# Kernel tuning notes

Measured on AMD Instinct MI355X. Metric: run time of the kernel, lower is better.

## Reference

```python
import jax, jax.numpy as jnp
import numpy as np

N, F, H, D = 4096, 128, 8, 8  # nodes, in_feat, head_num, att_embedding_size
EDGE_PROB = 0.01
NEG_INF = -1e10  # original uses -10e9 * (1 - A)


def setup_inputs() -> dict:
    key = jax.random.key(0)
    k1, k2, k3, k4, k5 = jax.random.split(key, 5)
    X = jax.random.normal(k1, (N, F), dtype=jnp.float32)
    # binary dense adjacency with self-loops (faithful to the dense-mask GAT formulation)
    A = (jax.random.uniform(k2, (N, N)) < EDGE_PROB).astype(jnp.float32)
    A = jnp.maximum(A, jnp.eye(N, dtype=jnp.float32))
    W = jax.random.normal(k3, (F, H * D), dtype=jnp.float32) * 0.05
    att_self = jax.random.normal(k4, (1, H, D), dtype=jnp.float32) * 0.05
    att_neigh = jax.random.normal(k5, (1, H, D), dtype=jnp.float32) * 0.05
    bias = jnp.zeros((1, H, D), dtype=jnp.float32)
    return {"X": X, "A": A, "W": W, "att_self": att_self,
            "att_neigh": att_neigh, "bias": bias}


def reference(X, A, W, att_self, att_neigh, bias):
    # per-head linear projection: [N, H, D]
    feats = (X @ W).reshape(N, H, D)
    # attention scores a_self^T h_i and a_neigh^T h_j : [N, H]
    a_s = jnp.sum(feats * att_self, axis=-1)
    a_n = jnp.sum(feats * att_neigh, axis=-1)
    # dense logits [H, N, N]: logits[h,i,j] = a_s[i,h] + a_n[j,h]
    logits = a_s.T[:, :, None] + a_n.T[:, None, :]
    logits = jax.nn.leaky_relu(logits, 0.2)
    logits = logits + NEG_INF * (1.0 - A)[None, :, :]
    attn = jax.nn.softmax(logits, axis=-1)  # [H, N, N]
    # weighted neighbor aggregation: [N, H, D]
    out = jnp.einsum('hij,jhd->ihd', attn, feats)
    out = out + bias  # use_bias=True
    out = out.reshape(N, H * D)  # reduction='concat'
    return jax.nn.relu(out)  # activation=relu
```

## Files before the change

kernel.cpp:

```cpp
#include <hip/hip_runtime.h>
#include <hip/hip_bf16.h>

#define NNODES 4096
#define FIN    128
#define NH     8
#define HD     8
#define HDOUT  64
#define MAXNZ  1024

typedef __hip_bfloat16 bf16;

template<typename T>
__device__ __forceinline__ float ld1(const void* p, int idx) {
    if constexpr (sizeof(T) == 2) return __bfloat162float(((const bf16*)p)[idx]);
    else                          return ((const float*)p)[idx];
}
template<typename T>
__device__ __forceinline__ void st1(void* p, int idx, float v) {
    if constexpr (sizeof(T) == 2) ((bf16*)p)[idx] = __float2bfloat16(v);
    else                          ((float*)p)[idx] = v;
}

__device__ __forceinline__ bool a_is_bf16(const void* A) {
    return ((*(const unsigned*)A) & 0xFFFFu) == 0x3F80u;
}

template<typename T>
__device__ __forceinline__ void proj_body(
    const void* X, const void* W, const void* att_s, const void* att_n,
    float* feats, float* a_s, float* a_n, int i, int t, float* xs)
{
    xs[t]      = ld1<T>(X, i * FIN + t);
    xs[t + 64] = ld1<T>(X, i * FIN + 64 + t);
    __syncthreads();

    float acc = 0.f;
    #pragma unroll 16
    for (int f = 0; f < FIN; ++f)
        acc += xs[f] * ld1<T>(W, f * HDOUT + t);

    feats[(size_t)i * HDOUT + t] = acc;

    float vs = acc * ld1<T>(att_s, t);
    float vn = acc * ld1<T>(att_n, t);
    #pragma unroll
    for (int m = 1; m < 8; m <<= 1) {
        vs += __shfl_xor(vs, m, 8);
        vn += __shfl_xor(vn, m, 8);
    }
    if ((t & 7) == 0) {
        a_s[i * NH + (t >> 3)] = vs;
        a_n[i * NH + (t >> 3)] = vn;
    }
}

__global__ __launch_bounds__(256) void k_proj(
    const void* __restrict__ A,
    const void* __restrict__ X, const void* __restrict__ W,
    const void* __restrict__ att_s, const void* __restrict__ att_n,
    float* __restrict__ feats, float* __restrict__ a_s, float* __restrict__ a_n)
{
    __shared__ float xs[4][FIN];
    const int w = threadIdx.x >> 6, t = threadIdx.x & 63;
    const int i = blockIdx.x * 4 + w;
    if (a_is_bf16(A)) proj_body<bf16 >(X, W, att_s, att_n, feats, a_s, a_n, i, t, xs[w]);
    else              proj_body<float>(X, W, att_s, att_n, feats, a_s, a_n, i, t, xs[w]);
}

template<typename T>
__device__ __forceinline__ void gat_body(
    const void* A, const float* feats, const float* a_s, const float* a_n,
    const void* bias, void* out, int i, int tid,
    int* s_cnt, int* s_idx, float (*s_num)[HDOUT], float (*s_den)[HDOUT])
{
    if (tid == 0) *s_cnt = 0;
    __syncthreads();

    #define FLUSH4(vx, vy, vz, vw, j0)                                            \
        do {                                                                      \
            if (vx) { int p = atomicAdd(s_cnt, 1); if (p < MAXNZ) s_idx[p] = (j0);     } \
            if (vy) { int p = atomicAdd(s_cnt, 1); if (p < MAXNZ) s_idx[p] = (j0) + 1; } \
            if (vz) { int p = atomicAdd(s_cnt, 1); if (p < MAXNZ) s_idx[p] = (j0) + 2; } \
            if (vw) { int p = atomicAdd(s_cnt, 1); if (p < MAXNZ) s_idx[p] = (j0) + 3; } \
        } while (0)

    if constexpr (sizeof(T) == 2) {
        const ushort4* Arow = (const ushort4*)((const bf16*)A + (size_t)i * NNODES);
        ushort4 v0 = Arow[tid];
        ushort4 v1 = Arow[256 + tid];
        ushort4 v2 = Arow[512 + tid];
        ushort4 v3 = Arow[768 + tid];
        FLUSH4(v0.x, v0.y, v0.z, v0.w, tid * 4);
        FLUSH4(v1.x, v1.y, v1.z, v1.w, (256 + tid) * 4);
        FLUSH4(v2.x, v2.y, v2.z, v2.w, (512 + tid) * 4);
        FLUSH4(v3.x, v3.y, v3.z, v3.w, (768 + tid) * 4);
    } else {
        const uint4* Arow = (const uint4*)((const float*)A + (size_t)i * NNODES);
        uint4 v0 = Arow[tid];
        uint4 v1 = Arow[256 + tid];
        uint4 v2 = Arow[512 + tid];
        uint4 v3 = Arow[768 + tid];
        FLUSH4(v0.x, v0.y, v0.z, v0.w, tid * 4);
        FLUSH4(v1.x, v1.y, v1.z, v1.w, (256 + tid) * 4);
        FLUSH4(v2.x, v2.y, v2.z, v2.w, (512 + tid) * 4);
        FLUSH4(v3.x, v3.y, v3.z, v3.w, (768 + tid) * 4);
    }
    #undef FLUSH4
    __syncthreads();
    int K = *s_cnt; if (K > MAXNZ) K = MAXNZ;

    const int rep = tid >> 6;
    const int u   = tid & 63;
    const int h   = u >> 3;
    const float ash = a_s[i * NH + h];

    float num = 0.f, den = 0.f;
    int k = rep;
    #pragma unroll 2
    for (; k + 4 < K; k += 8) {
        int ja = s_idx[k];
        int jb = s_idx[k + 4];
        float ana = a_n[ja * NH + h];
        float anb = a_n[jb * NH + h];
        float fa  = feats[(size_t)ja * HDOUT + u];
        float fb  = feats[(size_t)jb * HDOUT + u];
        float za = ash + ana; za = (za >= 0.f) ? za : 0.2f * za;
        float zb = ash + anb; zb = (zb >= 0.f) ? zb : 0.2f * zb;
        float ea = __expf(za);
        float eb = __expf(zb);
        num += ea * fa + eb * fb;
        den += ea + eb;
    }
    if (k < K) {
        int j = s_idx[k];
        float z = ash + a_n[j * NH + h];
        z = (z >= 0.f) ? z : 0.2f * z;
        float e = __expf(z);
        num += e * feats[(size_t)j * HDOUT + u];
        den += e;
    }
    s_num[rep][u] = num;
    s_den[rep][u] = den;
    __syncthreads();

    if (tid < HDOUT) {
        float n = s_num[0][u] + s_num[1][u] + s_num[2][u] + s_num[3][u];
        float d = s_den[0][u] + s_den[1][u] + s_den[2][u] + s_den[3][u];
        float v = n / d + ld1<T>(bias, u);
        st1<T>(out, i * HDOUT + u, fmaxf(v, 0.f));
    }
}

__global__ __launch_bounds__(256) void k_gat(
    const void* __restrict__ A, const float* __restrict__ feats,
    const float* __restrict__ a_s, const float* __restrict__ a_n,
    const void* __restrict__ bias, void* __restrict__ out)
{
    __shared__ int   s_cnt;
    __shared__ int   s_idx[MAXNZ];
    __shared__ float s_num[4][HDOUT];
    __shared__ float s_den[4][HDOUT];
    const int i = blockIdx.x, tid = threadIdx.x;
    if (a_is_bf16(A)) gat_body<bf16 >(A, feats, a_s, a_n, bias, out, i, tid, &s_cnt, s_idx, s_num, s_den);
    else              gat_body<float>(A, feats, a_s, a_n, bias, out, i, tid, &s_cnt, s_idx, s_num, s_den);
}

extern "C" void kernel_launch(void* const* d_in, const int* in_sizes, int n_in,
                              void* d_out, int out_size, void* d_ws, size_t ws_size,
                              hipStream_t stream) {
    const void* X     = d_in[0];
    const void* A     = d_in[1];
    const void* W     = d_in[2];
    const void* att_s = d_in[3];
    const void* att_n = d_in[4];
    const void* bias  = d_in[5];

    float* feats = (float*)d_ws;
    float* as_   = feats + (size_t)NNODES * HDOUT;
    float* an_   = as_   + (size_t)NNODES * NH;

    hipLaunchKernelGGL(k_proj, dim3(NNODES / 4), dim3(256), 0, stream,
                       A, X, W, att_s, att_n, feats, as_, an_);
    hipLaunchKernelGGL(k_gat,  dim3(NNODES), dim3(256), 0, stream,
                       A, feats, as_, an_, bias, d_out);
}
```

Before: 112.5 us.

## Fuse projection and aggregation into one cooperative kernel with async A-row prefetch

Merges the projection and attention-aggregation kernels into a single cooperative launch that uses a grid-wide sync between the phases. For bf16 adjacency it prefetches each block's four A rows into LDS with global_load_lds, so the row fetch overlaps the projection phase. Each block now handles four nodes, and the neighbour-index buffer is reduced to 512 entries. The cooperative launch needs all 1024 blocks resident at once, the grid sync adds its own cost, and the smaller MAXNZ means rows with more than 512 neighbours are silently truncated.

```diff
diff --git a/kernel.cpp b/kernel.cpp
--- a/kernel.cpp
+++ b/kernel.cpp
@@ -1,12 +1,16 @@
 #include <hip/hip_runtime.h>
 #include <hip/hip_bf16.h>
+#include <hip/hip_cooperative_groups.h>
+
+namespace cg = cooperative_groups;
 
 #define NNODES 4096
 #define FIN    128
 #define NH     8
 #define HD     8
 #define HDOUT  64
-#define MAXNZ  1024
+#define MAXNZ  512
+#define NODES_PER_BLK 4
 
 typedef __hip_bfloat16 bf16;
 
@@ -25,144 +29,167 @@
     return ((*(const unsigned*)A) & 0xFFFFu) == 0x3F80u;
 }
 
+typedef const __attribute__((address_space(1))) void* as1cvp;
+typedef __attribute__((address_space(3)))       void* as3vp;
+__device__ __forceinline__ void lds_stage16(void* lds, const void* g) {
+    __builtin_amdgcn_global_load_lds((as1cvp)g, (as3vp)lds, 16, 0, 0);
+}
+
+struct __align__(16) SharedMem {
+    unsigned char aRows[NODES_PER_BLK * NNODES * 2];
+    union {
+        float xs[NODES_PER_BLK][FIN];
+        struct {
+            int   idx[MAXNZ];
+            float num[4][HDOUT];
+            float den[4][HDOUT];
+        } p2;
+    } u;
+    int cnt;
+};
+
 template<typename T>
-__device__ __forceinline__ void proj_body(
-    const void* X, const void* W, const void* att_s, const void* att_n,
-    float* feats, float* a_s, float* a_n, int i, int t, float* xs)
+__device__ __forceinline__ void fused_body(
+    const void* A, const void* X, const void* W,
+    const void* att_s, const void* att_n, const void* bias,
+    void* out, float* feats, float* a_s, float* a_n, SharedMem& sm)
 {
-    xs[t]      = ld1<T>(X, i * FIN + t);
-    xs[t + 64] = ld1<T>(X, i * FIN + 64 + t);
+    const int tid = threadIdx.x;
+    const int w = tid >> 6, t = tid & 63;
+    const int i0 = blockIdx.x * NODES_PER_BLK;
+    const int i = i0 + w;
+
+    sm.u.xs[tid >> 7][tid & 127]         = ld1<T>(X, (i0 + (tid >> 7)) * FIN + (tid & 127));
+    sm.u.xs[2 + (tid >> 7)][tid & 127]   = ld1<T>(X, (i0 + 2 + (tid >> 7)) * FIN + (tid & 127));
+
+    if constexpr (sizeof(T) == 2) {
+        const char* Abase = (const char*)A + (size_t)i0 * NNODES * 2;
+        #pragma unroll
+        for (int it = 0; it < 8; ++it) {
+            const int chunk = w * 8 + it;
+            lds_stage16(sm.aRows + chunk * 1024, Abase + chunk * 1024 + t * 16);
+        }
+    }
     __syncthreads();
 
-    float acc = 0.f;
-    #pragma unroll 16
-    for (int f = 0; f < FIN; ++f)
-        acc += xs[f] * ld1<T>(W, f * HDOUT + t);
-
-    feats[(size_t)i * HDOUT + t] = acc;
-
-    float vs = acc * ld1<T>(att_s, t);
-    float vn = acc * ld1<T>(att_n, t);
-    #pragma unroll
-    for (int m = 1; m < 8; m <<= 1) {
-        vs += __shfl_xor(vs, m, 8);
-        vn += __shfl_xor(vn, m, 8);
+    {
+        const float* xs = sm.u.xs[w];
+        float acc = 0.f;
+        #pragma unroll 16
+        for (int f = 0; f < FIN; ++f)
+            acc += xs[f] * ld1<T>(W, f * HDOUT + t);
+
+        feats[(size_t)i * HDOUT + t] = acc;
+
+        float vs = acc * ld1<T>(att_s, t);
+        float vn = acc * ld1<T>(att_n, t);
+        #pragma unroll
+        for (int m = 1; m < 8; m <<= 1) {
+            vs += __shfl_xor(vs, m, 8);
+            vn += __shfl_xor(vn, m, 8);
+        }
+        if ((t & 7) == 0) {
+            a_s[i * NH + (t >> 3)] = vs;
+            a_n[i * NH + (t >> 3)] = vn;
+        }
     }
-    if ((t & 7) == 0) {
-        a_s[i * NH + (t >> 3)] = vs;
-        a_n[i * NH + (t >> 3)] = vn;
+
+    asm volatile("s_waitcnt vmcnt(0)" ::: "memory");
+    cg::this_grid().sync();
+
+    const int rep = w;
+    const int u   = t;
+    const int h   = u >> 3;
+
+    #define FLUSH4(vx, vy, vz, vw_, j0)                                               \
+        do {                                                                          \
+            if (vx)  { int p = atomicAdd(&sm.cnt, 1); if (p < MAXNZ) sm.u.p2.idx[p] = (j0);     } \
+            if (vy)  { int p = atomicAdd(&sm.cnt, 1); if (p < MAXNZ) sm.u.p2.idx[p] = (j0) + 1; } \
+            if (vz)  { int p = atomicAdd(&sm.cnt, 1); if (p < MAXNZ) sm.u.p2.idx[p] = (j0) + 2; } \
+            if (vw_) { int p = atomicAdd(&sm.cnt, 1); if (p < MAXNZ) sm.u.p2.idx[p] = (j0) + 3; } \
+        } while (0)
+
+    for (int n = 0; n < NODES_PER_BLK; ++n) {
+        const int node = i0 + n;
+        __syncthreads();
+        if (tid == 0) sm.cnt = 0;
+        __syncthreads();
+
+        if constexpr (sizeof(T) == 2) {
+            const ushort4* row = (const ushort4*)(sm.aRows + n * (NNODES * 2));
+            ushort4 v0 = row[tid];
+            ushort4 v1 = row[256 + tid];
+            ushort4 v2 = row[512 + tid];
+            ushort4 v3 = row[768 + tid];
+            FLUSH4(v0.x, v0.y, v0.z, v0.w, tid * 4);
+            FLUSH4(v1.x, v1.y, v1.z, v1.w, (256 + tid) * 4);
+            FLUSH4(v2.x, v2.y, v2.z, v2.w, (512 + tid) * 4);
+            FLUSH4(v3.x, v3.y, v3.z, v3.w, (768 + tid) * 4);
+        } else {
+            const uint4* Arow = (const uint4*)((const float*)A + (size_t)node * NNODES);
+            uint4 v0 = Arow[tid];
+            uint4 v1 = Arow[256 + tid];
+            uint4 v2 = Arow[512 + tid];
+            uint4 v3 = Arow[768 + tid];
+            FLUSH4(v0.x, v0.y, v0.z, v0.w, tid * 4);
+            FLUSH4(v1.x, v1.y, v1.z, v1.w, (256 + tid) * 4);
+            FLUSH4(v2.x, v2.y, v2.z, v2.w, (512 + tid) * 4);
+            FLUSH4(v3.x, v3.y, v3.z, v3.w, (768 + tid) * 4);
+        }
+        __syncthreads();
+        int K = sm.cnt; if (K > MAXNZ) K = MAXNZ;
+
+        const float ash = a_s[node * NH + h];
+        const int* idx = sm.u.p2.idx;
+
+        float num = 0.f, den = 0.f;
+        int k = rep;
+        #pragma unroll 2
+        for (; k + 4 < K; k += 8) {
+            int ja = idx[k];
+            int jb = idx[k + 4];
+            float ana = a_n[ja * NH + h];
+            float anb = a_n[jb * NH + h];
+            float fa  = feats[(size_t)ja * HDOUT + u];
+            float fb  = feats[(size_t)jb * HDOUT + u];
+            float za = ash + ana; za = (za >= 0.f) ? za : 0.2f * za;
+            float zb = ash + anb; zb = (zb >= 0.f) ? zb : 0.2f * zb;
+            float ea = __expf(za);
+            float eb = __expf(zb);
+            num += ea * fa + eb * fb;
+            den += ea + eb;
+        }
+        if (k < K) {
+            int j = idx[k];
+            float z = ash + a_n[j * NH + h];
+            z = (z >= 0.f) ? z : 0.2f * z;
+            float e = __expf(z);
+            num += e * feats[(size_t)j * HDOUT + u];
+            den += e;
+        }
+        sm.u.p2.num[rep][u] = num;
+        sm.u.p2.den[rep][u] = den;
+        __syncthreads();
+
+        if (tid < HDOUT) {
+            float nn = sm.u.p2.num[0][u] + sm.u.p2.num[1][u] + sm.u.p2.num[2][u] + sm.u.p2.num[3][u];
+            float dd = sm.u.p2.den[0][u] + sm.u.p2.den[1][u] + sm.u.p2.den[2][u] + sm.u.p2.den[3][u];
+            float v = nn / dd + ld1<T>(bias, u);
+            st1<T>(out, node * HDOUT + u, fmaxf(v, 0.f));
+        }
     }
-}
-
-__global__ __launch_bounds__(256) void k_proj(
-    const void* __restrict__ A,
-    const void* __restrict__ X, const void* __restrict__ W,
+    #undef FLUSH4
+}
+
+__global__ __launch_bounds__(256, 4) void k_fused(
+    const void* __restrict__ A, const void* __restrict__ X, const void* __restrict__ W,
     const void* __restrict__ att_s, const void* __restrict__ att_n,
+    const void* __restrict__ bias, void* __restrict__ out,
     float* __restrict__ feats, float* __restrict__ a_s, float* __restrict__ a_n)
 {
-    __shared__ float xs[4][FIN];
-    const int w = threadIdx.x >> 6, t = threadIdx.x & 63;
-    const int i = blockIdx.x * 4 + w;
-    if (a_is_bf16(A)) proj_body<bf16 >(X, W, att_s, att_n, feats, a_s, a_n, i, t, xs[w]);
-    else              proj_body<float>(X, W, att_s, att_n, feats, a_s, a_n, i, t, xs[w]);
-}
-
-template<typename T>
-__device__ __forceinline__ void gat_body(
-    const void* A, const float* feats, const float* a_s, const float* a_n,
-    const void* bias, void* out, int i, int tid,
-    int* s_cnt, int* s_idx, float (*s_num)[HDOUT], float (*s_den)[HDOUT])
-{
-    if (tid == 0) *s_cnt = 0;
-    __syncthreads();
-
-    #define FLUSH4(vx, vy, vz, vw, j0)                                            \
-        do {                                                                      \
-            if (vx) { int p = atomicAdd(s_cnt, 1); if (p < MAXNZ) s_idx[p] = (j0);     } \
-            if (vy) { int p = atomicAdd(s_cnt, 1); if (p < MAXNZ) s_idx[p] = (j0) + 1; } \
-            if (vz) { int p = atomicAdd(s_cnt, 1); if (p < MAXNZ) s_idx[p] = (j0) + 2; } \
-            if (vw) { int p = atomicAdd(s_cnt, 1); if (p < MAXNZ) s_idx[p] = (j0) + 3; } \
-        } while (0)
-
-    if constexpr (sizeof(T) == 2) {
-        const ushort4* Arow = (const ushort4*)((const bf16*)A + (size_t)i * NNODES);
-        ushort4 v0 = Arow[tid];
-        ushort4 v1 = Arow[256 + tid];
-        ushort4 v2 = Arow[512 + tid];
-        ushort4 v3 = Arow[768 + tid];
-        FLUSH4(v0.x, v0.y, v0.z, v0.w, tid * 4);
-        FLUSH4(v1.x, v1.y, v1.z, v1.w, (256 + tid) * 4);
-        FLUSH4(v2.x, v2.y, v2.z, v2.w, (512 + tid) * 4);
-        FLUSH4(v3.x, v3.y, v3.z, v3.w, (768 + tid) * 4);
-    } else {
-        const uint4* Arow = (const uint4*)((const float*)A + (size_t)i * NNODES);
-        uint4 v0 = Arow[tid];
-        uint4 v1 = Arow[256 + tid];
-        uint4 v2 = Arow[512 + tid];
-        uint4 v3 = Arow[768 + tid];
-        FLUSH4(v0.x, v0.y, v0.z, v0.w, tid * 4);
-        FLUSH4(v1.x, v1.y, v1.z, v1.w, (256 + tid) * 4);
-        FLUSH4(v2.x, v2.y, v2.z, v2.w, (512 + tid) * 4);
-        FLUSH4(v3.x, v3.y, v3.z, v3.w, (768 + tid) * 4);
-    }
-    #undef FLUSH4
-    __syncthreads();
-    int K = *s_cnt; if (K > MAXNZ) K = MAXNZ;
-
-    const int rep = tid >> 6;
-    const int u   = tid & 63;
-    const int h   = u >> 3;
-    const float ash = a_s[i * NH + h];
-
-    float num = 0.f, den = 0.f;
-    int k = rep;
-    #pragma unroll 2
-    for (; k + 4 < K; k += 8) {
-        int ja = s_idx[k];
-        int jb = s_idx[k + 4];
-        float ana = a_n[ja * NH + h];
-        float anb = a_n[jb * NH + h];
-        float fa  = feats[(size_t)ja * HDOUT + u];
-        float fb  = feats[(size_t)jb * HDOUT + u];
-        float za = ash + ana; za = (za >= 0.f) ? za : 0.2f * za;
-        float zb = ash + anb; zb = (zb >= 0.f) ? zb : 0.2f * zb;
-        float ea = __expf(za);
-        float eb = __expf(zb);
-        num += ea * fa + eb * fb;
-        den += ea + eb;
-    }
-    if (k < K) {
-        int j = s_idx[k];
-        float z = ash + a_n[j * NH + h];
-        z = (z >= 0.f) ? z : 0.2f * z;
-        float e = __expf(z);
-        num += e * feats[(size_t)j * HDOUT + u];
-        den += e;
-    }
-    s_num[rep][u] = num;
-    s_den[rep][u] = den;
-    __syncthreads();
-
-    if (tid < HDOUT) {
-        float n = s_num[0][u] + s_num[1][u] + s_num[2][u] + s_num[3][u];
-        float d = s_den[0][u] + s_den[1][u] + s_den[2][u] + s_den[3][u];
-        float v = n / d + ld1<T>(bias, u);
-        st1<T>(out, i * HDOUT + u, fmaxf(v, 0.f));
-    }
-}
-
-__global__ __launch_bounds__(256) void k_gat(
-    const void* __restrict__ A, const float* __restrict__ feats,
-    const float* __restrict__ a_s, const float* __restrict__ a_n,
-    const void* __restrict__ bias, void* __restrict__ out)
-{
-    __shared__ int   s_cnt;
-    __shared__ int   s_idx[MAXNZ];
-    __shared__ float s_num[4][HDOUT];
-    __shared__ float s_den[4][HDOUT];
-    const int i = blockIdx.x, tid = threadIdx.x;
-    if (a_is_bf16(A)) gat_body<bf16 >(A, feats, a_s, a_n, bias, out, i, tid, &s_cnt, s_idx, s_num, s_den);
-    else              gat_body<float>(A, feats, a_s, a_n, bias, out, i, tid, &s_cnt, s_idx, s_num, s_den);
+    __shared__ SharedMem sm;
+    if (a_is_bf16(A)) fused_body<bf16 >(A, X, W, att_s, att_n, bias, out, feats, a_s, a_n, sm);
+    else              fused_body<float>(A, X, W, att_s, att_n, bias, out, feats, a_s, a_n, sm);
 }
 
 extern "C" void kernel_launch(void* const* d_in, const int* in_sizes, int n_in,
@@ -179,8 +206,9 @@
     float* as_   = feats + (size_t)NNODES * HDOUT;
     float* an_   = as_   + (size_t)NNODES * NH;
 
-    hipLaunchKernelGGL(k_proj, dim3(NNODES / 4), dim3(256), 0, stream,
-                       A, X, W, att_s, att_n, feats, as_, an_);
-    hipLaunchKernelGGL(k_gat,  dim3(NNODES), dim3(256), 0, stream,
-                       A, feats, as_, an_, bias, d_out);
-}
+    void* kargs[] = {(void*)&A, (void*)&X, (void*)&W, (void*)&att_s, (void*)&att_n,
+                     (void*)&bias, (void*)&d_out, (void*)&feats, (void*)&as_, (void*)&an_};
+    hipLaunchCooperativeKernel((const void*)k_fused,
+                               dim3(NNODES / NODES_PER_BLK), dim3(256),
+                               kargs, 0, stream);
+}
```

Measured after the change: 252.8 us. 2.25x slower.

## Build per-row neighbor index lists in projection kernel via ballot-free bitmask prefix scan

Applied to the files above, without the earlier changes.

Moves the adjacency row scan out of the GAT kernel and into the projection kernel, where each wavefront compresses one row of A into a 64-bit mask per lane. A wave-level prefix scan then assigns output offsets, and the indices are written to a global CSR-like buffer. The GAT kernel just loads the compact index list, which removes the per-element shared-memory atomics and the dense row read from the critical aggregation kernel. The index order is now deterministic. MAXNZ drops to 512, so rows with more neighbours would be truncated, and the extra global index buffer adds traffic.

```diff
diff --git a/kernel.cpp b/kernel.cpp
--- a/kernel.cpp
+++ b/kernel.cpp
@@ -6,7 +6,8 @@
 #define NH     8
 #define HD     8
 #define HDOUT  64
-#define MAXNZ  1024
+#define MAXNZ  512
+#define NPB    4
 
 typedef __hip_bfloat16 bf16;
 
@@ -27,87 +28,103 @@
 
 template<typename T>
 __device__ __forceinline__ void proj_body(
-    const void* X, const void* W, const void* att_s, const void* att_n,
-    float* feats, float* a_s, float* a_n, int i, int t, float* xs)
-{
-    xs[t]      = ld1<T>(X, i * FIN + t);
-    xs[t + 64] = ld1<T>(X, i * FIN + 64 + t);
+    const void* A, const void* X, const void* W,
+    const void* att_s, const void* att_n,
+    float* feats, float* a_s, float* a_n, int* nz_cnt, int* nz_idx,
+    int i0, int w, int t, float (*xs)[FIN])
+{
+    const int tid = (w << 6) | t;
+
+    xs[tid >> 7][tid & 127]       = ld1<T>(X, (i0 +     (tid >> 7)) * FIN + (tid & 127));
+    xs[2 + (tid >> 7)][tid & 127] = ld1<T>(X, (i0 + 2 + (tid >> 7)) * FIN + (tid & 127));
     __syncthreads();
 
-    float acc = 0.f;
-    #pragma unroll 16
-    for (int f = 0; f < FIN; ++f)
-        acc += xs[f] * ld1<T>(W, f * HDOUT + t);
-
-    feats[(size_t)i * HDOUT + t] = acc;
-
-    float vs = acc * ld1<T>(att_s, t);
-    float vn = acc * ld1<T>(att_n, t);
+    const int i = i0 + w;
+
+    {
+        const float* x = xs[w];
+        float acc = 0.f;
+        #pragma unroll 16
+        for (int f = 0; f < FIN; ++f)
+            acc += x[f] * ld1<T>(W, f * HDOUT + t);
+
+        feats[(size_t)i * HDOUT + t] = acc;
+
+        float vs = acc * ld1<T>(att_s, t);
+        float vn = acc * ld1<T>(att_n, t);
+        #pragma unroll
+        for (int m = 1; m < 8; m <<= 1) {
+            vs += __shfl_xor(vs, m, 8);
+            vn += __shfl_xor(vn, m, 8);
+        }
+        if ((t & 7) == 0) {
+            a_s[i * NH + (t >> 3)] = vs;
+            a_n[i * NH + (t >> 3)] = vn;
+        }
+    }
+
+    unsigned long long m = 0ull;
+    if constexpr (sizeof(T) == 2) {
+        const ushort4* row = (const ushort4*)((const bf16*)A + (size_t)i * NNODES);
+        #pragma unroll
+        for (int it = 0; it < 16; ++it) {
+            ushort4 v = row[it * 64 + t];
+            unsigned nib = (v.x != 0) | ((v.y != 0) << 1) | ((v.z != 0) << 2) | ((v.w != 0) << 3);
+            m |= (unsigned long long)nib << (it * 4);
+        }
+    } else {
+        const uint4* row = (const uint4*)((const float*)A + (size_t)i * NNODES);
+        #pragma unroll
+        for (int it = 0; it < 16; ++it) {
+            uint4 v = row[it * 64 + t];
+            unsigned nib = (v.x != 0) | ((v.y != 0) << 1) | ((v.z != 0) << 2) | ((v.w != 0) << 3);
+            m |= (unsigned long long)nib << (it * 4);
+        }
+    }
+    int cnt = __popcll(m);
+
+    int inc = cnt;
     #pragma unroll
-    for (int m = 1; m < 8; m <<= 1) {
-        vs += __shfl_xor(vs, m, 8);
-        vn += __shfl_xor(vn, m, 8);
-    }
-    if ((t & 7) == 0) {
-        a_s[i * NH + (t >> 3)] = vs;
-        a_n[i * NH + (t >> 3)] = vn;
+    for (int d = 1; d < 64; d <<= 1) {
+        int o = __shfl_up(inc, d, 64);
+        if (t >= d) inc += o;
+    }
+    int off   = inc - cnt;
+    int total = __shfl(inc, 63, 64);
+    if (t == 0) nz_cnt[i] = (total < MAXNZ) ? total : MAXNZ;
+
+    int* dst = nz_idx + (size_t)i * MAXNZ;
+    while (m) {
+        int b = __ffsll((long long)m) - 1;
+        m &= m - 1;
+        if (off < MAXNZ)
+            dst[off++] = ((b >> 2) << 8) + (t << 2) + (b & 3);
     }
 }
 
 __global__ __launch_bounds__(256) void k_proj(
-    const void* __restrict__ A,
-    const void* __restrict__ X, const void* __restrict__ W,
+    const void* __restrict__ A, const void* __restrict__ X, const void* __restrict__ W,
     const void* __restrict__ att_s, const void* __restrict__ att_n,
-    float* __restrict__ feats, float* __restrict__ a_s, float* __restrict__ a_n)
-{
-    __shared__ float xs[4][FIN];
+    float* __restrict__ feats, float* __restrict__ a_s, float* __restrict__ a_n,
+    int* __restrict__ nz_cnt, int* __restrict__ nz_idx)
+{
+    __shared__ float xs[NPB][FIN];
     const int w = threadIdx.x >> 6, t = threadIdx.x & 63;
-    const int i = blockIdx.x * 4 + w;
-    if (a_is_bf16(A)) proj_body<bf16 >(X, W, att_s, att_n, feats, a_s, a_n, i, t, xs[w]);
-    else              proj_body<float>(X, W, att_s, att_n, feats, a_s, a_n, i, t, xs[w]);
+    const int i0 = blockIdx.x * NPB;
+    if (a_is_bf16(A)) proj_body<bf16 >(A, X, W, att_s, att_n, feats, a_s, a_n, nz_cnt, nz_idx, i0, w, t, xs);
+    else              proj_body<float>(A, X, W, att_s, att_n, feats, a_s, a_n, nz_cnt, nz_idx, i0, w, t, xs);
 }
 
 template<typename T>
 __device__ __forceinline__ void gat_body(
-    const void* A, const float* feats, const float* a_s, const float* a_n,
-    const void* bias, void* out, int i, int tid,
-    int* s_cnt, int* s_idx, float (*s_num)[HDOUT], float (*s_den)[HDOUT])
-{
-    if (tid == 0) *s_cnt = 0;
+    const int* nz_cnt, const int* nz_idx, const float* feats,
+    const float* a_s, const float* a_n, const void* bias, void* out,
+    int i, int tid, int* s_idx, float (*s_num)[HDOUT], float (*s_den)[HDOUT])
+{
+    const int K = nz_cnt[i];
+    for (int k = tid; k < K; k += 256)
+        s_idx[k] = nz_idx[(size_t)i * MAXNZ + k];
     __syncthreads();
-
-    #define FLUSH4(vx, vy, vz, vw, j0)                                            \
-        do {                                                                      \
-            if (vx) { int p = atomicAdd(s_cnt, 1); if (p < MAXNZ) s_idx[p] = (j0);     } \
-            if (vy) { int p = atomicAdd(s_cnt, 1); if (p < MAXNZ) s_idx[p] = (j0) + 1; } \
-            if (vz) { int p = atomicAdd(s_cnt, 1); if (p < MAXNZ) s_idx[p] = (j0) + 2; } \
-            if (vw) { int p = atomicAdd(s_cnt, 1); if (p < MAXNZ) s_idx[p] = (j0) + 3; } \
-        } while (0)
-
-    if constexpr (sizeof(T) == 2) {
-        const ushort4* Arow = (const ushort4*)((const bf16*)A + (size_t)i * NNODES);
-        ushort4 v0 = Arow[tid];
-        ushort4 v1 = Arow[256 + tid];
-        ushort4 v2 = Arow[512 + tid];
-        ushort4 v3 = Arow[768 + tid];
-        FLUSH4(v0.x, v0.y, v0.z, v0.w, tid * 4);
-        FLUSH4(v1.x, v1.y, v1.z, v1.w, (256 + tid) * 4);
-        FLUSH4(v2.x, v2.y, v2.z, v2.w, (512 + tid) * 4);
-        FLUSH4(v3.x, v3.y, v3.z, v3.w, (768 + tid) * 4);
-    } else {
-        const uint4* Arow = (const uint4*)((const float*)A + (size_t)i * NNODES);
-        uint4 v0 = Arow[tid];
-        uint4 v1 = Arow[256 + tid];
-        uint4 v2 = Arow[512 + tid];
-        uint4 v3 = Arow[768 + tid];
-        FLUSH4(v0.x, v0.y, v0.z, v0.w, tid * 4);
-        FLUSH4(v1.x, v1.y, v1.z, v1.w, (256 + tid) * 4);
-        FLUSH4(v2.x, v2.y, v2.z, v2.w, (512 + tid) * 4);
-        FLUSH4(v3.x, v3.y, v3.z, v3.w, (768 + tid) * 4);
-    }
-    #undef FLUSH4
-    __syncthreads();
-    int K = *s_cnt; if (K > MAXNZ) K = MAXNZ;
 
     const int rep = tid >> 6;
     const int u   = tid & 63;
@@ -152,17 +169,18 @@
 }
 
 __global__ __launch_bounds__(256) void k_gat(
-    const void* __restrict__ A, const float* __restrict__ feats,
-    const float* __restrict__ a_s, const float* __restrict__ a_n,
-    const void* __restrict__ bias, void* __restrict__ out)
-{
-    __shared__ int   s_cnt;
+    const void* __restrict__ A,
+    const int* __restrict__ nz_cnt, const int* __restrict__ nz_idx,
+    const float* __restrict__ feats, const float* __restrict__ a_s,
+    const float* __restrict__ a_n, const void* __restrict__ bias,
+    void* __restrict__ out)
+{
     __shared__ int   s_idx[MAXNZ];
     __shared__ float s_num[4][HDOUT];
     __shared__ float s_den[4][HDOUT];
     const int i = blockIdx.x, tid = threadIdx.x;
-    if (a_is_bf16(A)) gat_body<bf16 >(A, feats, a_s, a_n, bias, out, i, tid, &s_cnt, s_idx, s_num, s_den);
-    else              gat_body<float>(A, feats, a_s, a_n, bias, out, i, tid, &s_cnt, s_idx, s_num, s_den);
+    if (a_is_bf16(A)) gat_body<bf16 >(nz_cnt, nz_idx, feats, a_s, a_n, bias, out, i, tid, s_idx, s_num, s_den);
+    else              gat_body<float>(nz_cnt, nz_idx, feats, a_s, a_n, bias, out, i, tid, s_idx, s_num, s_den);
 }
 
 extern "C" void kernel_launch(void* const* d_in, const int* in_sizes, int n_in,
@@ -175,12 +193,14 @@
     const void* att_n = d_in[4];
     const void* bias  = d_in[5];
 
-    float* feats = (float*)d_ws;
-    float* as_   = feats + (size_t)NNODES * HDOUT;
-    float* an_   = as_   + (size_t)NNODES * NH;
-
-    hipLaunchKernelGGL(k_proj, dim3(NNODES / 4), dim3(256), 0, stream,
-                       A, X, W, att_s, att_n, feats, as_, an_);
+    float* feats  = (float*)d_ws;
+    float* as_    = feats + (size_t)NNODES * HDOUT;
+    float* an_    = as_   + (size_t)NNODES * NH;
+    int*   nz_cnt = (int*)(an_ + (size_t)NNODES * NH);
+    int*   nz_idx = nz_cnt + NNODES;
+
+    hipLaunchKernelGGL(k_proj, dim3(NNODES / NPB), dim3(256), 0, stream,
+                       A, X, W, att_s, att_n, feats, as_, an_, nz_cnt, nz_idx);
     hipLaunchKernelGGL(k_gat,  dim3(NNODES), dim3(256), 0, stream,
-                       A, feats, as_, an_, bias, d_out);
-}
+                       A, nz_cnt, nz_idx, feats, as_, an_, bias, d_out);
+}
```

After: 113.0 us. No clear change (+0.4%).
